# Performance work log

Hardware: AMD Instinct MI355X
Metric: run time of the kernel (lower is better)

The kernel has to match this reference:

```python
import jax, jax.numpy as jnp
import numpy as np

N, D = 8192, 128
TAU = 0.5
EPS = 1e-12  # F.normalize default eps


def setup_inputs() -> dict:
    key = jax.random.key(0)
    k = jax.random.split(key, 6)
    s = 1.0 / np.sqrt(D)  # torch Linear default init bound
    return {
        "z1": jax.random.normal(k[0], (N, D), dtype=jnp.float32),
        "z2": jax.random.normal(k[1], (N, D), dtype=jnp.float32),
        "w1": jax.random.uniform(k[2], (D, D), jnp.float32, -s, s),
        "b1": jax.random.uniform(k[3], (D,), jnp.float32, -s, s),
        "w2": jax.random.uniform(k[4], (D, D), jnp.float32, -s, s),
        "b2": jax.random.uniform(k[5], (D,), jnp.float32, -s, s),
    }


def _project(z, w1, b1, w2, b2):
    # fc2(elu(fc1(z))); torch Linear is x @ W.T + b
    h = jax.nn.elu(z @ w1.T + b1)
    return h @ w2.T + b2


def _normalize(z):
    n = jnp.linalg.norm(z, axis=1, keepdims=True)
    return z / jnp.maximum(n, EPS)


def _semi_loss(h1, h2):
    n1 = _normalize(h1)
    n2 = _normalize(h2)
    refl = jnp.exp((n1 @ n1.T) / TAU)   # [N, N]
    betw = jnp.exp((n1 @ n2.T) / TAU)   # [N, N]
    denom = refl.sum(axis=1) + betw.sum(axis=1) - jnp.diag(refl)
    return -jnp.log(jnp.diag(betw) / denom)


def reference(z1, z2, w1, b1, w2, b2):
    h1 = _project(z1, w1, b1, w2, b2)
    h2 = _project(z2, w1, b1, w2, b2)
    l1 = _semi_loss(h1, h2)
    l2 = _semi_loss(h2, h1)
    return ((l1 + l2) * 0.5).mean()
```

## Files before the change

kernel.cpp:

```cpp
#include <hip/hip_runtime.h>


#define NR 8192
#define DIM 128
#define SCALE_EXP2 2.885390081777927f
#define LOG2E 1.442695040888963f
#define LN2 0.6931471805599453f
#define E2 7.38905609893065f
#define NT 32

typedef __attribute__((ext_vector_type(8))) short short8;
typedef __attribute__((ext_vector_type(4))) float f32x4;
typedef __attribute__((ext_vector_type(16))) float f32x16;

__device__ unsigned short gN[2 * NR * DIM];
__device__ unsigned short gNs[2 * NR * DIM];
__device__ float gT[2 * NR];

__device__ inline float b2f(unsigned short h) {
    union { unsigned int u; float f; } x; x.u = ((unsigned int)h) << 16; return x.f;
}
__device__ inline unsigned short f2b(float f) {
    __bf16 h = (__bf16)f;
    unsigned short s;
    __builtin_memcpy(&s, &h, 2);
    return s;
}
__device__ inline short8 ldf8(const float* __restrict__ p) {
    f32x4 a = *(const f32x4*)p;
    f32x4 b = *(const f32x4*)(p + 4);
    short8 r;
#pragma unroll
    for (int j = 0; j < 4; ++j) r[j] = (short)f2b(a[j]);
#pragma unroll
    for (int j = 0; j < 4; ++j) r[4 + j] = (short)f2b(b[j]);
    return r;
}
__device__ inline f32x16 zero16() {
    f32x16 z;
#pragma unroll
    for (int i = 0; i < 16; ++i) z[i] = 0.0f;
    return z;
}
__device__ inline void gload_lds16(const void* g, void* l) {
    __builtin_amdgcn_global_load_lds(
        (const __attribute__((address_space(1))) unsigned int*)g,
        (__attribute__((address_space(3))) unsigned int*)l, 16, 0, 0);
}

__global__ __launch_bounds__(128) void k_proj(
        const float* __restrict__ Z1, const float* __restrict__ Z2,
        const float* __restrict__ W1, const float* __restrict__ B1,
        const float* __restrict__ W2, const float* __restrict__ B2,
        float* __restrict__ out) {
    __shared__ unsigned short hfrag[2][8][64][8];
    int t = threadIdx.x, w = t >> 6, l = t & 63;
    int lr = l & 31, lh = l >> 5;
    const float* Z = blockIdx.y ? Z2 : Z1;
    long rbase = (long)blockIdx.x * 64 + w * 32;

    int gi = ((int)blockIdx.y * 128 + (int)blockIdx.x) * 128 + t;
    if (gi < 2 * NR) gT[gi] = 0.0f;
    if (gi == 0) out[0] = 0.0f;

    short8 zf[8];
#pragma unroll
    for (int kc = 0; kc < 8; ++kc)
        zf[kc] = ldf8(Z + (rbase + lr) * DIM + kc * 16 + lh * 8);

#pragma unroll
    for (int tt = 0; tt < 4; ++tt) {
        short8 wf[8];
#pragma unroll
        for (int kc = 0; kc < 8; ++kc)
            wf[kc] = ldf8(W1 + (tt * 32 + lr) * DIM + kc * 16 + lh * 8);
        f32x16 a = zero16();
#pragma unroll
        for (int kc = 0; kc < 8; ++kc)
            a = __builtin_amdgcn_mfma_f32_32x32x16_bf16(zf[kc], wf[kc], a, 0, 0, 0);
        float bias = B1[tt * 32 + lr];
        int col = tt * 32 + lr;
#pragma unroll
        for (int r = 0; r < 16; ++r) {
            float v = a[r] + bias;
            if (v <= 0.0f) v = __builtin_amdgcn_exp2f(v * LOG2E) - 1.0f;
            int ro = (r & 3) + 8 * (r >> 2) + 4 * lh;
            hfrag[w][col >> 4][ro | (((col >> 3) & 1) << 5)][col & 7] = f2b(v);
        }
    }
    __syncthreads();

    short8 af[8];
#pragma unroll
    for (int kc = 0; kc < 8; ++kc)
        af[kc] = *(const short8*)&hfrag[w][kc][l][0];

    f32x16 acc[4];
#pragma unroll
    for (int tt = 0; tt < 4; ++tt) {
        short8 wf[8];
#pragma unroll
        for (int kc = 0; kc < 8; ++kc)
            wf[kc] = ldf8(W2 + (tt * 32 + lr) * DIM + kc * 16 + lh * 8);
        f32x16 a = zero16();
#pragma unroll
        for (int kc = 0; kc < 8; ++kc)
            a = __builtin_amdgcn_mfma_f32_32x32x16_bf16(af[kc], wf[kc], a, 0, 0, 0);
        float bias = B2[tt * 32 + lr];
#pragma unroll
        for (int r = 0; r < 16; ++r) a[r] += bias;
        acc[tt] = a;
    }
    float ss[16];
#pragma unroll
    for (int r = 0; r < 16; ++r)
        ss[r] = acc[0][r] * acc[0][r] + acc[1][r] * acc[1][r]
              + acc[2][r] * acc[2][r] + acc[3][r] * acc[3][r];
#pragma unroll
    for (int r = 0; r < 16; ++r) {
        ss[r] += __shfl_xor(ss[r], 1);  ss[r] += __shfl_xor(ss[r], 2);
        ss[r] += __shfl_xor(ss[r], 4);  ss[r] += __shfl_xor(ss[r], 8);
        ss[r] += __shfl_xor(ss[r], 16);
    }
    long nbase = (long)blockIdx.y * NR + rbase;
#pragma unroll
    for (int r = 0; r < 16; ++r) {
        float inv = 1.0f / fmaxf(sqrtf(ss[r]), 1e-12f);
        long row = nbase + (r & 3) + 8 * (r >> 2) + 4 * lh;
#pragma unroll
        for (int tt = 0; tt < 4; ++tt) {
            float v = acc[tt][r] * inv;
            gN[row * DIM + tt * 32 + lr]  = f2b(v);
            gNs[row * DIM + tt * 32 + lr] = f2b(v * SCALE_EXP2);
        }
    }
}

__global__ __launch_bounds__(256, 4) void k_sim() {
    __shared__ char smem[2 * 16384];
    int slice = blockIdx.x & 7, qp = blockIdx.x >> 3;
    int t = threadIdx.x, w = t >> 6, l = t & 63;
    int lr = l & 31, lh = l >> 5;
    long qbase = (long)qp * 128 + w * 32;
    long kb = (long)slice * 2048;

    short8 qf[8];
#pragma unroll
    for (int kc = 0; kc < 8; ++kc)
        qf[kc] = *(const short8*)(gNs + (qbase + lr) * DIM + kc * 16 + lh * 8);
    float rs[16];
#pragma unroll
    for (int r = 0; r < 16; ++r) rs[r] = 0.0f;

#define STAGE(BUF, TILE) do {                                                        \
    const unsigned short* _tb = gN + (kb + (long)(TILE) * 64) * DIM;                 \
    _Pragma("unroll")                                                                \
    for (int _c = 0; _c < 4; ++_c) {                                                 \
        int _i = _c * 256 + t;                                                       \
        int _j = (_i & ~15) | ((_i & 15) ^ ((_i >> 4) & 7));                         \
        gload_lds16(_tb + _j * 8, smem + (BUF) * 16384 + (_c * 4 + w) * 1024);       \
    }                                                                                \
} while (0)

    STAGE(0, 0);
    for (int tt = 0; tt < NT; ++tt) {
        int cur = tt & 1;
        if (tt + 1 < NT) {
            STAGE(cur ^ 1, tt + 1);
            asm volatile("s_waitcnt vmcnt(4)" ::: "memory");
        } else {
            asm volatile("s_waitcnt vmcnt(0)" ::: "memory");
        }
        __builtin_amdgcn_s_barrier();
        const char* bufp = smem + cur * 16384;
#pragma unroll
        for (int ks = 0; ks < 2; ++ks) {
            short8 bf[8];
#pragma unroll
            for (int kc = 0; kc < 8; ++kc) {
                int chunk = ((kc << 1) | lh) ^ (lr & 7);
                bf[kc] = *(const short8*)(bufp + (ks * 32 + lr) * 256 + chunk * 16);
            }
            f32x16 c = zero16();
#pragma unroll
            for (int kc = 0; kc < 8; ++kc)
                c = __builtin_amdgcn_mfma_f32_32x32x16_bf16(qf[kc], bf[kc], c, 0, 0, 0);
#pragma unroll
            for (int r = 0; r < 16; ++r)
                rs[r] += __builtin_amdgcn_exp2f(c[r]);
        }
        __builtin_amdgcn_s_barrier();
    }
#undef STAGE

#pragma unroll
    for (int r = 0; r < 16; ++r) {
        rs[r] += __shfl_xor(rs[r], 1);  rs[r] += __shfl_xor(rs[r], 2);
        rs[r] += __shfl_xor(rs[r], 4);  rs[r] += __shfl_xor(rs[r], 8);
        rs[r] += __shfl_xor(rs[r], 16);
    }
    if (lr == 0) {
#pragma unroll
        for (int r = 0; r < 16; ++r) {
            int ro = (r & 3) + 8 * (r >> 2) + 4 * lh;
            atomicAdd(&gT[qbase + ro], rs[r]);
        }
    }
}

__global__ __launch_bounds__(256) void k_loss(float* __restrict__ out) {
    int t = threadIdx.x, w = t >> 6, l = t & 63;
    int gw = blockIdx.x * 4 + w;
    float lsum = 0.0f;
    for (int row = gw; row < NR; row += 1024) {
        unsigned int pa = *(const unsigned int*)(gN + (long)row * DIM + l * 2);
        unsigned int pb = *(const unsigned int*)(gN + (long)(NR + row) * DIM + l * 2);
        float a0 = b2f((unsigned short)(pa & 0xFFFFu)), a1 = b2f((unsigned short)(pa >> 16));
        float b0 = b2f((unsigned short)(pb & 0xFFFFu)), b1 = b2f((unsigned short)(pb >> 16));
        float cr = a0 * b0 + a1 * b1;
#pragma unroll
        for (int off = 1; off < 64; off <<= 1)
            cr += __shfl_xor(cr, off);
        if (l == 0) {
            float d1 = gT[row]      - E2;
            float d2 = gT[NR + row] - E2;
            lsum += (__builtin_amdgcn_logf(d1) + __builtin_amdgcn_logf(d2)) * LN2 - 4.0f * cr;
        }
    }
    if (l == 0) atomicAdd(out, lsum * (0.5f / 8192.0f));
}

extern "C" void kernel_launch(void* const* d_in, const int* in_sizes, int n_in,
                              void* d_out, int out_size, void* d_ws, size_t ws_size,
                              hipStream_t stream) {
    const float* z1 = (const float*)d_in[0];
    const float* z2 = (const float*)d_in[1];
    const float* w1 = (const float*)d_in[2];
    const float* b1 = (const float*)d_in[3];
    const float* w2 = (const float*)d_in[4];
    const float* b2 = (const float*)d_in[5];

    k_proj<<<dim3(128, 2), 128, 0, stream>>>(z1, z2, w1, b1, w2, b2, (float*)d_out);
    k_sim<<<dim3(1024), 256, 0, stream>>>();
    k_loss<<<dim3(256), 256, 0, stream>>>((float*)d_out);
}
```

Measured before the change: 118.8 us.

## Exploit similarity matrix symmetry to compute only upper-triangular block tiles

```diff
diff --git a/kernel.cpp b/kernel.cpp
--- a/kernel.cpp
+++ b/kernel.cpp
@@ -138,11 +138,25 @@
 
 __global__ __launch_bounds__(256, 4) void k_sim() {
     __shared__ char smem[2 * 16384];
-    int slice = blockIdx.x & 7, qp = blockIdx.x >> 3;
+    __shared__ float colacc[2048];
+    int b = blockIdx.x;
+    int p, s, diag;
+    if (b < 128) { p = b; s = b >> 4; diag = 1; }
+    else {
+        int r = b - 128, g = 0;
+        for (;;) { int sz = 16 * (7 - g); if (r < sz) break; r -= sz; ++g; }
+        int within = 7 - g;
+        p = (g << 4) + r / within;
+        s = g + 1 + r % within;
+        diag = 0;
+    }
     int t = threadIdx.x, w = t >> 6, l = t & 63;
     int lr = l & 31, lh = l >> 5;
-    long qbase = (long)qp * 128 + w * 32;
-    long kb = (long)slice * 2048;
+    long qbase = (long)p * 128 + w * 32;
+    long kb = (long)s * 2048;
+
+    if (!diag)
+        for (int i = t; i < 2048; i += 256) colacc[i] = 0.0f;
 
     short8 qf[8];
 #pragma unroll
@@ -185,9 +199,18 @@
 #pragma unroll
             for (int kc = 0; kc < 8; ++kc)
                 c = __builtin_amdgcn_mfma_f32_32x32x16_bf16(qf[kc], bf[kc], c, 0, 0, 0);
-#pragma unroll
-            for (int r = 0; r < 16; ++r)
-                rs[r] += __builtin_amdgcn_exp2f(c[r]);
+            float cs = 0.0f;
+#pragma unroll
+            for (int r = 0; r < 16; ++r) {
+                float e = __builtin_amdgcn_exp2f(c[r]);
+                rs[r] += e;
+                cs += e;
+            }
+            if (!diag) {
+                cs += __shfl_xor(cs, 32);
+                if (l < 32)
+                    atomicAdd(&colacc[tt * 64 + ks * 32 + l], cs);
+            }
         }
         __builtin_amdgcn_s_barrier();
     }
@@ -205,6 +228,11 @@
             int ro = (r & 3) + 8 * (r >> 2) + 4 * lh;
             atomicAdd(&gT[qbase + ro], rs[r]);
         }
+    }
+    if (!diag) {
+        __syncthreads();
+        for (int i = t; i < 2048; i += 256)
+            atomicAdd(&gT[kb + i], colacc[i]);
     }
 }
 
@@ -241,6 +269,6 @@
     const float* b2 = (const float*)d_in[5];
 
     k_proj<<<dim3(128, 2), 128, 0, stream>>>(z1, z2, w1, b1, w2, b2, (float*)d_out);
-    k_sim<<<dim3(1024), 256, 0, stream>>>();
+    k_sim<<<dim3(576), 256, 0, stream>>>();
     k_loss<<<dim3(256), 256, 0, stream>>>((float*)d_out);
 }
```

Result: faster. 114.9 us (-3.2%).
